# Optimization experiments

Hardware: AMD Instinct MI355X
Metric: run time of the kernel (lower is better)

## Reference

```python
import jax, jax.numpy as jnp
import numpy as np

HEADS = 8
DIM_HEAD = 64
QUERY_DIM = 512
CONTEXT_DIM = 768
INNER = HEADS * DIM_HEAD  # 512


def setup_inputs() -> dict:
    key = jax.random.key(0)
    ks = jax.random.split(key, 8)
    s = lambda fan_in: 1.0 / np.sqrt(fan_in)
    return {
        "x": jax.random.normal(ks[0], (16, 4096, QUERY_DIM), dtype=jnp.float32),
        "context": jax.random.normal(ks[1], (16, 77, CONTEXT_DIM), dtype=jnp.float32),
        "ln_gamma": jnp.ones((QUERY_DIM,), dtype=jnp.float32),
        "ln_beta": jnp.zeros((QUERY_DIM,), dtype=jnp.float32),
        "Wq": jax.random.uniform(ks[2], (QUERY_DIM, INNER), jnp.float32, -s(QUERY_DIM), s(QUERY_DIM)),
        "Wk": jax.random.uniform(ks[3], (CONTEXT_DIM, INNER), jnp.float32, -s(CONTEXT_DIM), s(CONTEXT_DIM)),
        "Wv": jax.random.uniform(ks[4], (CONTEXT_DIM, INNER), jnp.float32, -s(CONTEXT_DIM), s(CONTEXT_DIM)),
        "Wo": jax.random.uniform(ks[5], (INNER, QUERY_DIM), jnp.float32, -s(INNER), s(INNER)),
        "bo": jax.random.uniform(ks[6], (QUERY_DIM,), jnp.float32, -s(INNER), s(INNER)),
    }


def _layernorm(x, gamma, beta, eps=1e-5):
    mu = jnp.mean(x, axis=-1, keepdims=True)
    var = jnp.mean((x - mu) ** 2, axis=-1, keepdims=True)
    return (x - mu) * jax.lax.rsqrt(var + eps) * gamma + beta


def reference(x, context, ln_gamma, ln_beta, Wq, Wk, Wv, Wo, bo):
    B, N, D = x.shape
    scale = DIM_HEAD ** -0.5
    h = _layernorm(x, ln_gamma, ln_beta)
    # project then split heads: [B, H, S, d]
    q = (h @ Wq).reshape(B, N, HEADS, DIM_HEAD).transpose(0, 2, 1, 3)
    M = context.shape[1]
    k = (context @ Wk).reshape(B, M, HEADS, DIM_HEAD).transpose(0, 2, 1, 3)
    v = (context @ Wv).reshape(B, M, HEADS, DIM_HEAD).transpose(0, 2, 1, 3)
    scores = jnp.einsum("bhnd,bhmd->bhnm", q, k) * scale
    attn = jax.nn.softmax(scores, axis=-1)
    out = jnp.einsum("bhnm,bhmd->bhnd", attn, v)  # [B,H,N,d]
    out = out.transpose(0, 2, 1, 3).reshape(B, N, INNER)
    return x + out @ Wo + bo
```

## Files before the change

### kernel.cpp

```cpp
#include <hip/hip_runtime.h>


#define DQ 512
#define DC 768
#define MCTX 77
#define MPAD 96
#define DH 64

typedef __attribute__((ext_vector_type(8))) short bf16x8;
typedef __attribute__((ext_vector_type(4))) short s16x4;
typedef __attribute__((ext_vector_type(4))) float f32x4;
typedef __attribute__((ext_vector_type(16))) float f32x16;

__device__ __forceinline__ short f2bf(float f) {
    unsigned u = __builtin_bit_cast(unsigned, f);
    u = (u + 0x7FFFu + ((u >> 16) & 1u)) >> 16;
    return (short)u;
}
__device__ __forceinline__ unsigned cvtpk(float lo, float hi) {
    unsigned r;
    asm("v_cvt_pk_bf16_f32 %0, %1, %2" : "=v"(r) : "v"(lo), "v"(hi));
    return r;
}

#define SWZ(row, byte) ((byte) ^ (((row) & 7) << 4))
#define MFMA(a, b, c) __builtin_amdgcn_mfma_f32_16x16x32_bf16((a), (b), (c), 0, 0, 0)
#define MFMA32(a, b, c) __builtin_amdgcn_mfma_f32_32x32x16_bf16((a), (b), (c), 0, 0, 0)

__global__ void transpose_cast(const float* __restrict__ src, short* __restrict__ dst,
                               int K, int N) {
    __shared__ float t[32][33];
    int ntn = N >> 5;
    int tn = blockIdx.x % ntn, tk = blockIdx.x / ntn;
    int tx = threadIdx.x & 31, ty = threadIdx.x >> 5;
#pragma unroll
    for (int i = 0; i < 32; i += 8)
        t[ty + i][tx] = src[(size_t)(tk * 32 + ty + i) * N + tn * 32 + tx];
    __syncthreads();
#pragma unroll
    for (int i = 0; i < 32; i += 8)
        dst[(size_t)(tn * 32 + ty + i) * K + tk * 32 + tx] = f2bf(t[tx][ty + i]);
}

__global__ void pack_frag32(const float* __restrict__ src, short* __restrict__ dst,
                            int K, int N) {
    int idx = blockIdx.x * 256 + threadIdx.x;
    int lane = idx & 63;
    int chunk = idx >> 6;
    int NT = N >> 5;
    int t = chunk % NT, ks = chunk / NT;
    if (ks * 16 >= K) return;
    int n = t * 32 + (lane & 31);
    int k0 = ks * 16 + (lane >> 5) * 8;
    bf16x8 v;
#pragma unroll
    for (int j = 0; j < 8; ++j) v[j] = f2bf(src[(size_t)(k0 + j) * N + n]);
    *(bf16x8*)(dst + (size_t)idx * 8) = v;
}

__global__ __launch_bounds__(256, 1) void kv_proj(const float* __restrict__ ctxin,
                                                  const short* __restrict__ WkT,
                                                  const short* __restrict__ WvT,
                                                  short* __restrict__ Kb,
                                                  short* __restrict__ VbT) {
    int b = blockIdx.x >> 2;
    int kv = (blockIdx.x >> 1) & 1;
    int half = blockIdx.x & 1;
    const short* WT = kv ? WvT : WkT;

    __shared__ short A[48 * 768];
    const int tid = threadIdx.x;
    const int lane = tid & 63, wv = tid >> 6;
    const int l15 = lane & 15, l4 = lane >> 4;

#pragma unroll
    for (int it = 0; it < 36; ++it) {
        int id = it * 256 + tid;
        int row = id / 192, col = (id % 192) * 4;
        int gctx = half * 48 + row;
        float4 v = make_float4(0.f, 0.f, 0.f, 0.f);
        if (gctx < MCTX)
            v = ((const float4*)(ctxin + ((size_t)(b * MCTX + gctx)) * DC))[id % 192];
        s16x4 s4;
        s4[0] = f2bf(v.x); s4[1] = f2bf(v.y); s4[2] = f2bf(v.z); s4[3] = f2bf(v.w);
        *(s16x4*)((char*)A + row * 1536 + SWZ(row, col * 2)) = s4;
    }
    __syncthreads();

    f32x4 zf = {0.f, 0.f, 0.f, 0.f};
    f32x4 acc[3][8];
#pragma unroll
    for (int m = 0; m < 3; ++m)
#pragma unroll
        for (int nb = 0; nb < 8; ++nb) acc[m][nb] = zf;

    for (int ks = 0; ks < 24; ++ks) {
        bf16x8 bb[8], aa[3];
#pragma unroll
        for (int nb = 0; nb < 8; ++nb) {
            int n = wv * 128 + nb * 16 + l15;
            bb[nb] = *(const bf16x8*)((const char*)WT + (size_t)n * 1536 + ks * 64 + l4 * 16);
        }
#pragma unroll
        for (int m = 0; m < 3; ++m) {
            int row = m * 16 + l15;
            aa[m] = *(const bf16x8*)((char*)A + row * 1536 + SWZ(row, ks * 64 + l4 * 16));
        }
#pragma unroll
        for (int nb = 0; nb < 8; ++nb)
#pragma unroll
            for (int m = 0; m < 3; ++m) acc[m][nb] = MFMA(aa[m], bb[nb], acc[m][nb]);
    }

    if (kv == 0) {
#pragma unroll
        for (int m = 0; m < 3; ++m)
#pragma unroll
            for (int nb = 0; nb < 8; ++nb)
#pragma unroll
                for (int r = 0; r < 4; ++r) {
                    int ctxi = half * 48 + m * 16 + l4 * 4 + r;
                    int col = wv * 128 + nb * 16 + l15;
                    Kb[((size_t)(b * MPAD + ctxi)) * 512 + col] = f2bf(acc[m][nb][r]);
                }
    } else {
#pragma unroll
        for (int m = 0; m < 3; ++m)
#pragma unroll
            for (int nb = 0; nb < 8; ++nb)
#pragma unroll
                for (int r = 0; r < 4; ++r) {
                    int ctxi = half * 48 + m * 16 + l4 * 4 + r;
                    int col = wv * 128 + nb * 16 + l15;
                    VbT[((size_t)(b * 512 + col)) * MPAD + ctxi] = f2bf(acc[m][nb][r]);
                }
    }
}

__global__ __launch_bounds__(512, 4) void fused_attn(
    const float* __restrict__ x, const float* __restrict__ gamma,
    const float* __restrict__ beta, const short* __restrict__ WqF,
    const short* __restrict__ WoF, const short* __restrict__ Kb,
    const short* __restrict__ VbT, const float* __restrict__ bo,
    float* __restrict__ out) {
    __shared__ short A[64 * 512];

    const int tid = threadIdx.x;
    const int lane = tid & 63, wv = tid >> 6;
    const int l15 = lane & 15, l4 = lane >> 4;
    const int l31 = lane & 31, hi5 = lane >> 5;
    const int swz = (blockIdx.x & 7) * 128 + (blockIdx.x >> 3);
    const int b = swz >> 6;
    const size_t rowbase = (size_t)swz * 64;
    const int cb = wv * 64;

    {
        float g[8], be[8];
        float4 g0 = ((const float4*)gamma)[lane * 2], g1 = ((const float4*)gamma)[lane * 2 + 1];
        float4 b0 = ((const float4*)beta)[lane * 2], b1 = ((const float4*)beta)[lane * 2 + 1];
        g[0] = g0.x; g[1] = g0.y; g[2] = g0.z; g[3] = g0.w;
        g[4] = g1.x; g[5] = g1.y; g[6] = g1.z; g[7] = g1.w;
        be[0] = b0.x; be[1] = b0.y; be[2] = b0.z; be[3] = b0.w;
        be[4] = b1.x; be[5] = b1.y; be[6] = b1.z; be[7] = b1.w;
#pragma unroll 1
        for (int g4 = 0; g4 < 2; ++g4) {
            float4 v0[4], v1[4];
#pragma unroll
            for (int j = 0; j < 4; ++j) {
                int row = wv * 8 + g4 * 4 + j;
                const float4* xp = (const float4*)(x + (rowbase + row) * DQ);
                v0[j] = xp[lane * 2];
                v1[j] = xp[lane * 2 + 1];
            }
#pragma unroll
            for (int j = 0; j < 4; ++j) {
                int row = wv * 8 + g4 * 4 + j;
                float vv[8] = {v0[j].x, v0[j].y, v0[j].z, v0[j].w,
                               v1[j].x, v1[j].y, v1[j].z, v1[j].w};
                float s = 0.f, s2 = 0.f;
#pragma unroll
                for (int i = 0; i < 8; ++i) { s += vv[i]; s2 = fmaf(vv[i], vv[i], s2); }
#pragma unroll
                for (int m = 1; m < 64; m <<= 1) {
                    s += __shfl_xor(s, m);
                    s2 += __shfl_xor(s2, m);
                }
                float mu = s * (1.f / 512.f);
                float var = s2 * (1.f / 512.f) - mu * mu;
                float rs = rsqrtf(var + 1e-5f);
                float hn[8];
#pragma unroll
                for (int i = 0; i < 8; ++i) hn[i] = (vv[i] - mu) * rs * g[i] + be[i];
                uint4 hv = make_uint4(cvtpk(hn[0], hn[1]), cvtpk(hn[2], hn[3]),
                                      cvtpk(hn[4], hn[5]), cvtpk(hn[6], hn[7]));
                *(uint4*)((char*)A + row * 1024 + SWZ(row, lane * 16)) = hv;
            }
        }
    }

    f32x4 zf = {0.f, 0.f, 0.f, 0.f};

#define LDWF(dst, W, ks)                                                                   \
    _Pragma("unroll") for (int tt = 0; tt < 2; ++tt) {                                     \
        (dst)[tt] = *(const bf16x8*)((W) +                                                 \
            (size_t)((((ks)*16 + wv * 2 + tt) * 64 + lane)) * 8);                          \
    }
#define LDT32(dst, ks)                                                                     \
    _Pragma("unroll") for (int tt = 0; tt < 2; ++tt) {                                     \
        int row = tt * 32 + l31;                                                           \
        (dst)[tt] = *(const bf16x8*)((char*)A + row * 1024 +                               \
                                     SWZ(row, (ks)*32 + hi5 * 16));                        \
    }
#define GSTEP_Q(W, ACC, WBASE, kk)                                                         \
    {                                                                                      \
        bf16x8 hb[2];                                                                      \
        LDT32(hb, (kk));                                                                   \
        _Pragma("unroll") for (int mt = 0; mt < 2; ++mt)                                   \
            _Pragma("unroll") for (int nt = 0; nt < 2; ++nt)                               \
                ACC[mt][nt] = MFMA32((W)[mt], hb[nt], ACC[mt][nt]);                        \
        LDWF((W), (WBASE), (kk) + 4);                                                      \
    }
#define GSTEP_Q_NR(W, ACC, kk)                                                             \
    {                                                                                      \
        bf16x8 hb[2];                                                                      \
        LDT32(hb, (kk));                                                                   \
        _Pragma("unroll") for (int mt = 0; mt < 2; ++mt)                                   \
            _Pragma("unroll") for (int nt = 0; nt < 2; ++nt)                               \
                ACC[mt][nt] = MFMA32((W)[mt], hb[nt], ACC[mt][nt]);                        \
    }
#define GSTEP_O(W, ACC, WBASE, kk)                                                         \
    {                                                                                      \
        bf16x8 hb[2];                                                                      \
        LDT32(hb, (kk));                                                                   \
        _Pragma("unroll") for (int mt = 0; mt < 2; ++mt)                                   \
            _Pragma("unroll") for (int ct = 0; ct < 2; ++ct)                               \
                ACC[mt][ct] = MFMA32(hb[mt], (W)[ct], ACC[mt][ct]);                        \
        LDWF((W), (WBASE), (kk) + 4);                                                      \
    }
#define GSTEP_O_NR(W, ACC, kk)                                                             \
    {                                                                                      \
        bf16x8 hb[2];                                                                      \
        LDT32(hb, (kk));                                                                   \
        _Pragma("unroll") for (int mt = 0; mt < 2; ++mt)                                   \
            _Pragma("unroll") for (int ct = 0; ct < 2; ++ct)                               \
                ACC[mt][ct] = MFMA32(hb[mt], (W)[ct], ACC[mt][ct]);                        \
    }

    {
        bf16x8 w0[2], w1[2], w2[2], w3[2];
        LDWF(w0, WqF, 0);
        LDWF(w1, WqF, 1);
        LDWF(w2, WqF, 2);
        LDWF(w3, WqF, 3);
        __syncthreads();

        f32x16 qa[2][2];
#pragma unroll
        for (int mt = 0; mt < 2; ++mt)
#pragma unroll
            for (int nt = 0; nt < 2; ++nt)
#pragma unroll
                for (int i = 0; i < 16; ++i) qa[mt][nt][i] = 0.f;

#pragma unroll 1
        for (int ks = 0; ks < 28; ks += 4) {
            GSTEP_Q(w0, qa, WqF, ks)
            GSTEP_Q(w1, qa, WqF, ks + 1)
            GSTEP_Q(w2, qa, WqF, ks + 2)
            GSTEP_Q(w3, qa, WqF, ks + 3)
        }
        GSTEP_Q_NR(w0, qa, 28)
        GSTEP_Q_NR(w1, qa, 29)
        GSTEP_Q_NR(w2, qa, 30)
        GSTEP_Q_NR(w3, qa, 31)
        __syncthreads();

#pragma unroll
        for (int mt = 0; mt < 2; ++mt)
#pragma unroll
            for (int nt = 0; nt < 2; ++nt)
#pragma unroll
                for (int g = 0; g < 4; ++g) {
                    uint2 qv = make_uint2(
                        cvtpk(qa[mt][nt][g * 4] * 0.125f, qa[mt][nt][g * 4 + 1] * 0.125f),
                        cvtpk(qa[mt][nt][g * 4 + 2] * 0.125f, qa[mt][nt][g * 4 + 3] * 0.125f));
                    int row = nt * 32 + l31;
                    int colb = (cb + mt * 32 + 8 * g + 4 * hi5) * 2;
                    *(uint2*)((char*)A + row * 1024 + SWZ(row, colb)) = qv;
                }
    }

    {
        const int srcA = ((l4 & 1) << 5) + l15;
        const int srcB = srcA + 16;
        const bool hi = (l4 >> 1) != 0;

        bf16x8 vR[3][4];
#pragma unroll
        for (int ks = 0; ks < 3; ++ks)
#pragma unroll
            for (int nb = 0; nb < 4; ++nb)
                vR[ks][nb] = *(const bf16x8*)(VbT +
                                              ((size_t)(b * 512 + cb + nb * 16 + l15)) * MPAD +
                                              ks * 32 + l4 * 8);

#pragma unroll 1
        for (int rp = 0; rp < 4; ++rp) {
            bf16x8 qf0, qf1;
            {
                int qrow = rp * 16 + l15;
                qf0 = *(const bf16x8*)((char*)A + qrow * 1024 + SWZ(qrow, cb * 2 + l4 * 16));
                qf1 = *(const bf16x8*)((char*)A + qrow * 1024 + SWZ(qrow, cb * 2 + 64 + l4 * 16));
            }
            f32x4 sc[5];
            __builtin_amdgcn_s_setprio(1);
#pragma unroll
            for (int f = 0; f < 5; ++f) {
                bf16x8 k0 = *(const bf16x8*)(Kb + ((size_t)(b * MPAD + f * 16 + l15)) * 512 +
                                             cb + l4 * 8);
                bf16x8 k1 = *(const bf16x8*)(Kb + ((size_t)(b * MPAD + f * 16 + l15)) * 512 +
                                             cb + 32 + l4 * 8);
                sc[f] = MFMA(k0, qf0, zf);
                sc[f] = MFMA(k1, qf1, sc[f]);
            }
            __builtin_amdgcn_s_setprio(0);
            float m = -1e30f;
#pragma unroll
            for (int f = 0; f < 5; ++f)
#pragma unroll
                for (int r = 0; r < 4; ++r) {
                    float v = sc[f][r];
                    if (f == 4 && (64 + l4 * 4 + r) >= MCTX) v = -1e30f;
                    sc[f][r] = v;
                    m = fmaxf(m, v);
                }
            m = fmaxf(m, __shfl_xor(m, 16));
            m = fmaxf(m, __shfl_xor(m, 32));
            float s = 0.f;
#pragma unroll
            for (int f = 0; f < 5; ++f)
#pragma unroll
                for (int r = 0; r < 4; ++r) {
                    float p = __expf(sc[f][r] - m);
                    sc[f][r] = p;
                    s += p;
                }
            s += __shfl_xor(s, 16);
            s += __shfl_xor(s, 32);
            float inv = 1.f / s;
            unsigned pk[6][2];
#pragma unroll
            for (int f = 0; f < 5; ++f) {
                pk[f][0] = cvtpk(sc[f][0] * inv, sc[f][1] * inv);
                pk[f][1] = cvtpk(sc[f][2] * inv, sc[f][3] * inv);
            }
            pk[5][0] = 0; pk[5][1] = 0;
            unsigned pa[3][4];
#pragma unroll
            for (int ks = 0; ks < 3; ++ks) {
                unsigned aL0 = __shfl((int)pk[2 * ks][0], srcA);
                unsigned aL1 = __shfl((int)pk[2 * ks][1], srcA);
                unsigned aH0 = __shfl((int)pk[2 * ks + 1][0], srcA);
                unsigned aH1 = __shfl((int)pk[2 * ks + 1][1], srcA);
                unsigned bL0 = __shfl((int)pk[2 * ks][0], srcB);
                unsigned bL1 = __shfl((int)pk[2 * ks][1], srcB);
                unsigned bH0 = __shfl((int)pk[2 * ks + 1][0], srcB);
                unsigned bH1 = __shfl((int)pk[2 * ks + 1][1], srcB);
                pa[ks][0] = hi ? aH0 : aL0;
                pa[ks][1] = hi ? aH1 : aL1;
                pa[ks][2] = hi ? bH0 : bL0;
                pa[ks][3] = hi ? bH1 : bL1;
            }
            f32x4 ov[4];
#pragma unroll
            for (int nb = 0; nb < 4; ++nb) ov[nb] = zf;
            __builtin_amdgcn_s_setprio(1);
#pragma unroll
            for (int ks = 0; ks < 3; ++ks) {
                bf16x8 ap = __builtin_bit_cast(bf16x8, pa[ks]);
#pragma unroll
                for (int nb = 0; nb < 4; ++nb) {
                    ov[nb] = MFMA(vR[ks][nb], ap, ov[nb]);
                }
            }
            __builtin_amdgcn_s_setprio(0);
#pragma unroll
            for (int nb = 0; nb < 4; ++nb) {
                uint2 av = make_uint2(cvtpk(ov[nb][0], ov[nb][1]),
                                      cvtpk(ov[nb][2], ov[nb][3]));
                int row = rp * 16 + l15;
                int colb = (cb + nb * 16 + l4 * 4) * 2;
                *(uint2*)((char*)A + row * 1024 + SWZ(row, colb)) = av;
            }
        }
    }

    {
        bf16x8 w0[2], w1[2], w2[2], w3[2];
        LDWF(w0, WoF, 0);
        LDWF(w1, WoF, 1);
        LDWF(w2, WoF, 2);
        LDWF(w3, WoF, 3);
        __syncthreads();

        f32x16 oa[2][2];
#pragma unroll
        for (int mt = 0; mt < 2; ++mt)
#pragma unroll
            for (int ct = 0; ct < 2; ++ct)
#pragma unroll
                for (int i = 0; i < 16; ++i) oa[mt][ct][i] = 0.f;

#pragma unroll 1
        for (int ks = 0; ks < 28; ks += 4) {
            GSTEP_O(w0, oa, WoF, ks)
            GSTEP_O(w1, oa, WoF, ks + 1)
            GSTEP_O(w2, oa, WoF, ks + 2)
            GSTEP_O(w3, oa, WoF, ks + 3)
        }
        GSTEP_O_NR(w0, oa, 28)
        GSTEP_O_NR(w1, oa, 29)
        GSTEP_O_NR(w2, oa, 30)
        GSTEP_O_NR(w3, oa, 31)

#pragma unroll
        for (int mt = 0; mt < 2; ++mt)
#pragma unroll
            for (int ct = 0; ct < 2; ++ct) {
                int col = cb + ct * 32 + l31;
                float bov = bo[col];
                float xv[16];
#pragma unroll
                for (int rg = 0; rg < 16; ++rg) {
                    int row = mt * 32 + (rg & 3) + 8 * (rg >> 2) + 4 * hi5;
                    xv[rg] = x[(rowbase + row) * DQ + col];
                }
#pragma unroll
                for (int rg = 0; rg < 16; ++rg) {
                    int row = mt * 32 + (rg & 3) + 8 * (rg >> 2) + 4 * hi5;
                    size_t gi = (rowbase + row) * DQ + col;
                    out[gi] = xv[rg] + oa[mt][ct][rg] + bov;
                }
            }
    }
}

extern "C" void kernel_launch(void* const* d_in, const int* in_sizes, int n_in,
                              void* d_out, int out_size, void* d_ws, size_t ws_size,
                              hipStream_t stream) {
    const float* x = (const float*)d_in[0];
    const float* ctx = (const float*)d_in[1];
    const float* gamma = (const float*)d_in[2];
    const float* beta = (const float*)d_in[3];
    const float* Wq = (const float*)d_in[4];
    const float* Wk = (const float*)d_in[5];
    const float* Wv = (const float*)d_in[6];
    const float* Wo = (const float*)d_in[7];
    const float* bo = (const float*)d_in[8];
    float* out = (float*)d_out;

    char* ws = (char*)d_ws;
    short* WqF = (short*)(ws + 0);
    short* WkT = (short*)(ws + 524288);
    short* WvT = (short*)(ws + 1310720);
    short* WoF = (short*)(ws + 2097152);
    short* Kb = (short*)(ws + 2621440);
    short* VbT = (short*)(ws + 4194304);

    pack_frag32<<<128, 256, 0, stream>>>(Wq, WqF, 512, 512);
    transpose_cast<<<384, 256, 0, stream>>>(Wk, WkT, 768, 512);
    transpose_cast<<<384, 256, 0, stream>>>(Wv, WvT, 768, 512);
    pack_frag32<<<128, 256, 0, stream>>>(Wo, WoF, 512, 512);
    kv_proj<<<64, 256, 0, stream>>>(ctx, WkT, WvT, Kb, VbT);
    fused_attn<<<1024, 512, 0, stream>>>(x, gamma, beta, WqF, WoF, Kb, VbT, bo, out);
}
```

Measured before the change: 197.1 us.

## Merge weight prep kernels and stream V fragments inside the PV loop

Four weight-conversion launches (pack Wq/Wo, transpose-cast Wk/Wv) become one prep_weights kernel that picks its branch from the block index, which removes three launch gaps. In the fused attention kernel the 12 V fragments are no longer preloaded into registers before the row loop. They are now loaded from global memory just before each PV MFMA, lowering register pressure at the cost of reloading V on every row-pass. This trades register use for extra global/L2 traffic and load latency inside the inner loop.

```diff
diff --git a/kernel.cpp b/kernel.cpp
--- a/kernel.cpp
+++ b/kernel.cpp
@@ -27,35 +27,40 @@
 #define MFMA(a, b, c) __builtin_amdgcn_mfma_f32_16x16x32_bf16((a), (b), (c), 0, 0, 0)
 #define MFMA32(a, b, c) __builtin_amdgcn_mfma_f32_32x32x16_bf16((a), (b), (c), 0, 0, 0)
 
-__global__ void transpose_cast(const float* __restrict__ src, short* __restrict__ dst,
-                               int K, int N) {
+__global__ void prep_weights(const float* __restrict__ Wq, const float* __restrict__ Wk,
+                             const float* __restrict__ Wv, const float* __restrict__ Wo,
+                             short* __restrict__ WqF, short* __restrict__ WkT,
+                             short* __restrict__ WvT, short* __restrict__ WoF) {
     __shared__ float t[32][33];
-    int ntn = N >> 5;
-    int tn = blockIdx.x % ntn, tk = blockIdx.x / ntn;
-    int tx = threadIdx.x & 31, ty = threadIdx.x >> 5;
-#pragma unroll
-    for (int i = 0; i < 32; i += 8)
-        t[ty + i][tx] = src[(size_t)(tk * 32 + ty + i) * N + tn * 32 + tx];
-    __syncthreads();
-#pragma unroll
-    for (int i = 0; i < 32; i += 8)
-        dst[(size_t)(tn * 32 + ty + i) * K + tk * 32 + tx] = f2bf(t[tx][ty + i]);
-}
-
-__global__ void pack_frag32(const float* __restrict__ src, short* __restrict__ dst,
-                            int K, int N) {
-    int idx = blockIdx.x * 256 + threadIdx.x;
-    int lane = idx & 63;
-    int chunk = idx >> 6;
-    int NT = N >> 5;
-    int t = chunk % NT, ks = chunk / NT;
-    if (ks * 16 >= K) return;
-    int n = t * 32 + (lane & 31);
-    int k0 = ks * 16 + (lane >> 5) * 8;
-    bf16x8 v;
-#pragma unroll
-    for (int j = 0; j < 8; ++j) v[j] = f2bf(src[(size_t)(k0 + j) * N + n]);
-    *(bf16x8*)(dst + (size_t)idx * 8) = v;
+    int bid = blockIdx.x;
+    if (bid < 256) {
+        const float* src = (bid < 128) ? Wq : Wo;
+        short* dst = (bid < 128) ? WqF : WoF;
+        int vb = bid & 127;
+        int idx = vb * 256 + threadIdx.x;
+        int lane = idx & 63;
+        int chunk = idx >> 6;
+        int tt = chunk % 16, ks = chunk / 16;
+        int n = tt * 32 + (lane & 31);
+        int k0 = ks * 16 + (lane >> 5) * 8;
+        bf16x8 v;
+#pragma unroll
+        for (int j = 0; j < 8; ++j) v[j] = f2bf(src[(size_t)(k0 + j) * 512 + n]);
+        *(bf16x8*)(dst + (size_t)idx * 8) = v;
+    } else {
+        const float* src = (bid < 640) ? Wk : Wv;
+        short* dst = (bid < 640) ? WkT : WvT;
+        int vb = (bid - 256) % 384;
+        int tn = vb % 16, tk = vb / 16;
+        int tx = threadIdx.x & 31, ty = threadIdx.x >> 5;
+#pragma unroll
+        for (int i = 0; i < 32; i += 8)
+            t[ty + i][tx] = src[(size_t)(tk * 32 + ty + i) * 512 + tn * 32 + tx];
+        __syncthreads();
+#pragma unroll
+        for (int i = 0; i < 32; i += 8)
+            dst[(size_t)(tn * 32 + ty + i) * 768 + tk * 32 + tx] = f2bf(t[tx][ty + i]);
+    }
 }
 
 __global__ __launch_bounds__(256, 1) void kv_proj(const float* __restrict__ ctxin,
@@ -295,15 +300,6 @@
         const int srcB = srcA + 16;
         const bool hi = (l4 >> 1) != 0;
 
-        bf16x8 vR[3][4];
-#pragma unroll
-        for (int ks = 0; ks < 3; ++ks)
-#pragma unroll
-            for (int nb = 0; nb < 4; ++nb)
-                vR[ks][nb] = *(const bf16x8*)(VbT +
-                                              ((size_t)(b * 512 + cb + nb * 16 + l15)) * MPAD +
-                                              ks * 32 + l4 * 8);
-
 #pragma unroll 1
         for (int rp = 0; rp < 4; ++rp) {
             bf16x8 qf0, qf1;
@@ -355,7 +351,10 @@
                 pk[f][1] = cvtpk(sc[f][2] * inv, sc[f][3] * inv);
             }
             pk[5][0] = 0; pk[5][1] = 0;
-            unsigned pa[3][4];
+
+            f32x4 ov[4];
+#pragma unroll
+            for (int nb = 0; nb < 4; ++nb) ov[nb] = zf;
 #pragma unroll
             for (int ks = 0; ks < 3; ++ks) {
                 unsigned aL0 = __shfl((int)pk[2 * ks][0], srcA);
@@ -366,24 +365,22 @@
                 unsigned bL1 = __shfl((int)pk[2 * ks][1], srcB);
                 unsigned bH0 = __shfl((int)pk[2 * ks + 1][0], srcB);
                 unsigned bH1 = __shfl((int)pk[2 * ks + 1][1], srcB);
-                pa[ks][0] = hi ? aH0 : aL0;
-                pa[ks][1] = hi ? aH1 : aL1;
-                pa[ks][2] = hi ? bH0 : bL0;
-                pa[ks][3] = hi ? bH1 : bL1;
-            }
-            f32x4 ov[4];
-#pragma unroll
-            for (int nb = 0; nb < 4; ++nb) ov[nb] = zf;
-            __builtin_amdgcn_s_setprio(1);
-#pragma unroll
-            for (int ks = 0; ks < 3; ++ks) {
-                bf16x8 ap = __builtin_bit_cast(bf16x8, pa[ks]);
+                unsigned paw[4];
+                paw[0] = hi ? aH0 : aL0;
+                paw[1] = hi ? aH1 : aL1;
+                paw[2] = hi ? bH0 : bL0;
+                paw[3] = hi ? bH1 : bL1;
+                bf16x8 ap = __builtin_bit_cast(bf16x8, paw);
+                __builtin_amdgcn_s_setprio(1);
 #pragma unroll
                 for (int nb = 0; nb < 4; ++nb) {
-                    ov[nb] = MFMA(vR[ks][nb], ap, ov[nb]);
-                }
-            }
-            __builtin_amdgcn_s_setprio(0);
+                    bf16x8 bv = *(const bf16x8*)(VbT +
+                                                 ((size_t)(b * 512 + cb + nb * 16 + l15)) * MPAD +
+                                                 ks * 32 + l4 * 8);
+                    ov[nb] = MFMA(bv, ap, ov[nb]);
+                }
+                __builtin_amdgcn_s_setprio(0);
+            }
 #pragma unroll
             for (int nb = 0; nb < 4; ++nb) {
                 uint2 av = make_uint2(cvtpk(ov[nb][0], ov[nb][1]),
@@ -467,10 +464,7 @@
     short* Kb = (short*)(ws + 2621440);
     short* VbT = (short*)(ws + 4194304);
 
-    pack_frag32<<<128, 256, 0, stream>>>(Wq, WqF, 512, 512);
-    transpose_cast<<<384, 256, 0, stream>>>(Wk, WkT, 768, 512);
-    transpose_cast<<<384, 256, 0, stream>>>(Wv, WvT, 768, 512);
-    pack_frag32<<<128, 256, 0, stream>>>(Wo, WoF, 512, 512);
+    prep_weights<<<1024, 256, 0, stream>>>(Wq, Wk, Wv, Wo, WqF, WkT, WvT, WoF);
     kv_proj<<<64, 256, 0, stream>>>(ctx, WkT, WvT, Kb, VbT);
     fused_attn<<<1024, 512, 0, stream>>>(x, gamma, beta, WqF, WoF, Kb, VbT, bo, out);
 }
```

Result: no change. 195.7 us (-0.7%).
